# Kernel optimization log

Measured on AMD Instinct MI355X. Metric: run time of the kernel, lower is better.

## Reference

```python
import jax, jax.numpy as jnp
import numpy as np

N, F, E = 65536, 64, 16   # batch, fields, embedding_size
H1, H2 = 8, 4             # hidden_dims
BN_EPS = 1e-5


def setup_inputs() -> dict:
    key = jax.random.key(0)
    ks = jax.random.split(key, 12)
    rn = lambda k, shape, sc=1.0: jax.random.normal(k, shape, dtype=jnp.float32) * sc
    return {
        "Xa": rn(ks[0], (N, F)),
        "Xc": rn(ks[1], (N, F)),
        # per-field Linear(1,1) weights/biases (two first-order embedding lists)
        "w1": rn(ks[2], (F,)), "b1": rn(ks[3], (F,)),
        "w2": rn(ks[4], (F,)), "b2": rn(ks[5], (F,)),
        # per-field Linear(1,E) weights/biases (two second-order embedding lists)
        "W1": rn(ks[6], (F, E)), "B1": rn(ks[7], (F, E)),
        "W2": rn(ks[8], (F, E)), "B2": rn(ks[9], (F, E)),
        # deep MLP: linear_1 (F*E -> 8) + BN, linear_2 (8 -> 4). No final layer (init bug).
        "lin1_w": rn(ks[10], (H1, F * E), 0.01), "lin1_b": jnp.zeros((H1,), jnp.float32),
        "bn1_gamma": jnp.ones((H1,), jnp.float32), "bn1_beta": jnp.zeros((H1,), jnp.float32),
        "lin2_w": rn(ks[11], (H2, H1), 0.01), "lin2_b": jnp.full((H2,), 0.21, jnp.float32),
    }


def reference(Xa, Xc, w1, b1, w2, b2, W1, B1, W2, B2,
              lin1_w, lin1_b, bn1_gamma, bn1_beta, lin2_w, lin2_b):
    n = Xa.shape[0]
    # ---- FM first order (faithful to the torch broadcast: arr_2[i] is (N,N)
    # with entry [r,c] = Xa[r,i]*(w2[i]*Xc[c,i]+b2[i]); only mean over the
    # concat dim is consumed, so compute the column-mean analytically). ----
    first1 = (w1 * Xa + b1) * Xc                         # (N,F)
    xc_mean = jnp.mean(Xc, axis=0)                       # (F,)
    first2_cmean = Xa * (w2 * xc_mean + b2)              # (N,F) = mean over c of arr_2
    fm_first_mean = jnp.mean(first1 + first2_cmean, axis=1, keepdims=True)  # (N,1)

    # ---- FM second order: per-field (N,E) embeddings, fully batched. ----
    Xa3 = Xa[:, :, None]                                 # (N,F,1)
    Xc3 = Xc[:, :, None]
    emb = (Xa3 * W1 + B1) * Xc3 + Xa3 * (W2 * Xc3 + B2)  # (N,F,E)
    s = emb.sum(axis=1)                                  # (N,E)
    fm_second = 0.5 * (s * s - (emb * emb).sum(axis=1))  # (N,E)
    fm_second_mean = jnp.mean(fm_second, axis=1, keepdims=True)  # (N,1)

    # ---- deep part: cat of per-field (N,E) -> (N, F*E), field-major. ----
    deep = emb.reshape(n, F * E)
    h = deep @ lin1_w.T + lin1_b                         # (N,8)
    mu = h.mean(axis=0)
    var = h.var(axis=0)                                  # biased, as BN training mode
    h = (h - mu) / jnp.sqrt(var + BN_EPS) * bn1_gamma + bn1_beta
    h = jnp.tanh(h)                                      # dropout = identity (eval)
    h = h @ lin2_w.T + lin2_b                            # (N,4) — no final projection (init bug)
    deep_mean = h.mean(axis=1, keepdims=True)            # (N,1)

    return fm_first_mean + fm_second_mean + deep_mean    # (N,1)
```

## Files before the change

kernel.cpp:

```cpp
#include <hip/hip_runtime.h>
#include <math.h>

#define NROWS 65536
#define BN_EPS 1e-5f
#define NBLK   512

#define OFF_PARTIAL 0
#define OFF_H       65536
#define OFF_REC     589824
#define OFF_BLKT    595200
#define OFF_T       636160

__global__ __launch_bounds__(64) void precompute_kernel(
    const float* __restrict__ W1, const float* __restrict__ B1,
    const float* __restrict__ W2, const float* __restrict__ B2,
    const float* __restrict__ lin1_w, const float* __restrict__ w1,
    const float* __restrict__ b1, const float* __restrict__ b2,
    float* __restrict__ rec)
{
    int f = blockIdx.x, t = threadIdx.x;
    __shared__ float u[16], x[16], y[16];
    if (t < 16) {
        float uu = W1[f * 16 + t] + W2[f * 16 + t];
        float xx = B1[f * 16 + t];
        float yy = B2[f * 16 + t];
        u[t] = uu; x[t] = xx; y[t] = yy;
        rec[f * 84 + t]      = uu;
        rec[f * 84 + 16 + t] = xx;
        rec[f * 84 + 32 + t] = yy;
    }
    __syncthreads();
    if (t < 24) {
        int j = t & 7, which = t >> 3;
        const float* src = (which == 0) ? u : (which == 1) ? x : y;
        const float* lw = lin1_w + j * 1024 + f * 16;
        float acc = 0.f;
#pragma unroll
        for (int e = 0; e < 16; e++) acc = fmaf(src[e], lw[e], acc);
        rec[f * 84 + 48 + which * 8 + j] = acc;
    } else if (t < 30) {
        int q = t - 24;
        const float* s1 = (q == 0 || q == 3 || q == 4) ? u : (q == 1 || q == 5) ? x : y;
        const float* s2 = (q == 0) ? u : (q == 1 || q == 3) ? x : y;
        float acc = 0.f;
#pragma unroll
        for (int e = 0; e < 16; e++) acc = fmaf(s1[e], s2[e], acc);
        rec[f * 84 + 72 + q] = (q < 3 ? 1.f : 2.f) * acc;
    } else if (t == 30) {
        rec[f * 84 + 78] = w1[f];
        rec[f * 84 + 79] = b1[f];
        rec[f * 84 + 80] = b2[f];
        rec[f * 84 + 81] = 0.f;
        rec[f * 84 + 82] = 0.f;
        rec[f * 84 + 83] = 0.f;
    }
}

__global__ __launch_bounds__(256, 4) void main_kernel(
    const float* __restrict__ Xa, const float* __restrict__ Xc,
    const float* __restrict__ rec, const float* __restrict__ lin1_b,
    float* __restrict__ ws_partial, float* __restrict__ ws_h,
    float* __restrict__ ws_blkT)
{
    __shared__ float cmb[4][64][29];
    __shared__ float scol[256];

    int tid  = threadIdx.x;
    int lane = tid & 63;
    int wv   = tid >> 6;
    int wu   = __builtin_amdgcn_readfirstlane(wv);
    int blk  = blockIdx.x;
    int f0   = wu * 16;
    int rowbase = blk * 128;

    {
        int col = tid & 63, grp = tid >> 6;
        float acc = 0.f;
        for (int r = grp; r < 128; r += 4)
            acc += Xc[(size_t)(rowbase + r) * 64 + col];
        scol[tid] = acc;
    }
    __syncthreads();
    if (tid < 64) {
        float t = scol[tid] + scol[64 + tid] + scol[128 + tid] + scol[192 + tid];
        ws_blkT[(size_t)tid * NBLK + blk] = t;
    }

    size_t rb0 = ((size_t)rowbase + lane) * 64 + f0;
    const float4* pa0 = (const float4*)(Xa + rb0);
    const float4* pc0 = (const float4*)(Xc + rb0);
    const float4* pa1 = (const float4*)(Xa + rb0 + 64 * 64);
    const float4* pc1 = (const float4*)(Xc + rb0 + 64 * 64);

    float s0[16], s1[16], h0[8], h1[8];
#pragma unroll
    for (int e = 0; e < 16; e++) { s0[e] = 0.f; s1[e] = 0.f; }
#pragma unroll
    for (int j = 0; j < 8; j++) { h0[j] = 0.f; h1[j] = 0.f; }
    float p1a = 0.f, p1b = 0.f, p2a0 = 0.f, p2a1 = 0.f, q0 = 0.f, q1 = 0.f;

    const float* recw = rec + (size_t)f0 * 84;
#pragma unroll
    for (int k = 0; k < 4; k++) {
        float4 A0 = pa0[k], C0 = pc0[k];
        float4 A1 = pa1[k], C1 = pc1[k];
        float av0[4] = {A0.x, A0.y, A0.z, A0.w};
        float cv0[4] = {C0.x, C0.y, C0.z, C0.w};
        float av1[4] = {A1.x, A1.y, A1.z, A1.w};
        float cv1[4] = {C1.x, C1.y, C1.z, C1.w};
#pragma unroll
        for (int uu = 0; uu < 4; uu++) {
            const float* r = recw + (k * 4 + uu) * 84;
            {
                float a = av0[uu], c = cv0[uu], pp = a * c;
                p1a  = fmaf(fmaf(r[78], a, r[79]), c, p1a);
                p2a0 = fmaf(a, r[80], p2a0);
                q0 = fmaf(pp * pp, r[72], q0);
                q0 = fmaf(c * c,   r[73], q0);
                q0 = fmaf(a * a,   r[74], q0);
                q0 = fmaf(pp * c,  r[75], q0);
                q0 = fmaf(pp * a,  r[76], q0);
                q0 = fmaf(pp,      r[77], q0);
#pragma unroll
                for (int e = 0; e < 16; e++)
                    s0[e] = fmaf(pp, r[e], fmaf(c, r[16+e], fmaf(a, r[32+e], s0[e])));
#pragma unroll
                for (int j = 0; j < 8; j++)
                    h0[j] = fmaf(pp, r[48+j], fmaf(c, r[56+j], fmaf(a, r[64+j], h0[j])));
            }
            {
                float a = av1[uu], c = cv1[uu], pp = a * c;
                p1b  = fmaf(fmaf(r[78], a, r[79]), c, p1b);
                p2a1 = fmaf(a, r[80], p2a1);
                q1 = fmaf(pp * pp, r[72], q1);
                q1 = fmaf(c * c,   r[73], q1);
                q1 = fmaf(a * a,   r[74], q1);
                q1 = fmaf(pp * c,  r[75], q1);
                q1 = fmaf(pp * a,  r[76], q1);
                q1 = fmaf(pp,      r[77], q1);
#pragma unroll
                for (int e = 0; e < 16; e++)
                    s1[e] = fmaf(pp, r[e], fmaf(c, r[16+e], fmaf(a, r[32+e], s1[e])));
#pragma unroll
                for (int j = 0; j < 8; j++)
                    h1[j] = fmaf(pp, r[48+j], fmaf(c, r[56+j], fmaf(a, r[64+j], h1[j])));
            }
        }
    }

    float bn[16];
#pragma unroll
    for (int i = 0; i < 16; i++) bn[i] = 0.f;

#pragma unroll
    for (int g = 0; g < 2; g++) {
        __syncthreads();
#pragma unroll
        for (int e = 0; e < 16; e++) cmb[wv][lane][e] = g ? s1[e] : s0[e];
#pragma unroll
        for (int j = 0; j < 8; j++) cmb[wv][lane][16 + j] = g ? h1[j] : h0[j];
        cmb[wv][lane][24] = g ? p1b : p1a;
        cmb[wv][lane][25] = g ? p2a1 : p2a0;
        cmb[wv][lane][26] = g ? q1 : q0;
        __syncthreads();

        if (tid < 64) {
            float S[16], H[8], P1 = 0.f, P2 = 0.f, Q = 0.f;
#pragma unroll
            for (int e = 0; e < 16; e++) S[e] = 0.f;
#pragma unroll
            for (int j = 0; j < 8; j++) H[j] = 0.f;
#pragma unroll
            for (int w = 0; w < 4; w++) {
#pragma unroll
                for (int e = 0; e < 16; e++) S[e] += cmb[w][tid][e];
#pragma unroll
                for (int j = 0; j < 8; j++) H[j] += cmb[w][tid][16 + j];
                P1 += cmb[w][tid][24];
                P2 += cmb[w][tid][25];
                Q  += cmb[w][tid][26];
            }
#pragma unroll
            for (int j = 0; j < 8; j++) H[j] += lin1_b[j];

            float ss = 0.f;
#pragma unroll
            for (int e = 0; e < 16; e++) ss = fmaf(S[e], S[e], ss);
            int rr = rowbase + g * 64 + tid;
            ws_partial[rr] = (P1 + P2) * (1.f / 64.f) + (ss - Q) * (0.5f / 16.f);
            *(float4*)(ws_h + (size_t)rr * 8)     = make_float4(H[0], H[1], H[2], H[3]);
            *(float4*)(ws_h + (size_t)rr * 8 + 4) = make_float4(H[4], H[5], H[6], H[7]);
#pragma unroll
            for (int j = 0; j < 8; j++) {
                bn[j]     += H[j];
                bn[8 + j] += H[j] * H[j];
            }
        }
    }

    if (tid < 64) {
#pragma unroll
        for (int off = 1; off < 64; off <<= 1) {
#pragma unroll
            for (int i = 0; i < 16; i++) bn[i] += __shfl_xor(bn[i], off);
        }
        if (tid == 0) {
#pragma unroll
            for (int i = 0; i < 16; i++)
                ws_blkT[(size_t)(64 + i) * NBLK + blk] = bn[i];
        }
    }
}

__global__ __launch_bounds__(256) void reduce_kernel(
    const float* __restrict__ ws_blkT, float* __restrict__ T)
{
    int gtid = blockIdx.x * 256 + threadIdx.x;
    int v = gtid >> 6;
    int lane = gtid & 63;
    const float* p = ws_blkT + (size_t)v * NBLK + lane;
    float acc = 0.f;
#pragma unroll
    for (int k = 0; k < 8; k++) acc += p[k * 64];
#pragma unroll
    for (int off = 32; off; off >>= 1) acc += __shfl_xor(acc, off);
    if (lane == 0) T[v] = acc;
}

__global__ __launch_bounds__(256) void final_kernel(
    const float* __restrict__ Xa, const float* __restrict__ w2,
    const float* __restrict__ gamma, const float* __restrict__ beta,
    const float* __restrict__ lin2_w, const float* __restrict__ lin2_b,
    const float* __restrict__ T, const float* __restrict__ ws_partial,
    const float* __restrict__ ws_h, float* __restrict__ out)
{
    __shared__ float sg[64], sScale[8], sShift[8], sColw[8];
    __shared__ float sBsum;
    int tid = threadIdx.x;
    if (tid < 64) {
        sg[tid] = w2[tid] * (T[tid] * (1.f / 65536.f));
    } else if (tid < 72) {
        int j = tid - 64;
        float mu  = T[64 + j] * (1.f / 65536.f);
        float var = T[72 + j] * (1.f / 65536.f) - mu * mu;
        float sc = gamma[j] / sqrtf(var + BN_EPS);
        sScale[j] = sc;
        sShift[j] = beta[j] - mu * sc;
    } else if (tid < 80) {
        int j = tid - 72;
        sColw[j] = lin2_w[j] + lin2_w[8 + j] + lin2_w[16 + j] + lin2_w[24 + j];
    } else if (tid == 80) {
        sBsum = lin2_b[0] + lin2_b[1] + lin2_b[2] + lin2_b[3];
    }
    __syncthreads();

    int row  = (blockIdx.x * 256 + tid) >> 1;
    int half = tid & 1;
    int fo   = half * 32;

    const float4* xa4 = (const float4*)(Xa + (size_t)row * 64 + fo);
    float p2b = 0.f;
#pragma unroll
    for (int k = 0; k < 8; k++) {
        float4 vv = xa4[k];
        int b = fo + k * 4;
        p2b += vv.x * sg[b] + vv.y * sg[b + 1] + vv.z * sg[b + 2] + vv.w * sg[b + 3];
    }

    float4 hq = *(const float4*)(ws_h + (size_t)row * 8 + half * 4);
    float hv[4] = {hq.x, hq.y, hq.z, hq.w};
    float dmp = 0.f;
#pragma unroll
    for (int jj = 0; jj < 4; jj++) {
        int j = half * 4 + jj;
        float hn = tanhf(hv[jj] * sScale[j] + sShift[j]);
        dmp = fmaf(hn, sColw[j], dmp);
    }

    float val = p2b * (1.f / 64.f) + dmp * 0.25f;
    val += __shfl_xor(val, 1);
    if (!half)
        out[row] = val + ws_partial[row] + sBsum * 0.25f;
}

extern "C" void kernel_launch(void* const* d_in, const int* in_sizes, int n_in,
                              void* d_out, int out_size, void* d_ws, size_t ws_size,
                              hipStream_t stream) {
    const float* Xa        = (const float*)d_in[0];
    const float* Xc        = (const float*)d_in[1];
    const float* w1        = (const float*)d_in[2];
    const float* b1        = (const float*)d_in[3];
    const float* w2        = (const float*)d_in[4];
    const float* b2        = (const float*)d_in[5];
    const float* W1        = (const float*)d_in[6];
    const float* B1        = (const float*)d_in[7];
    const float* W2        = (const float*)d_in[8];
    const float* B2        = (const float*)d_in[9];
    const float* lin1_w    = (const float*)d_in[10];
    const float* lin1_b    = (const float*)d_in[11];
    const float* bn1_gamma = (const float*)d_in[12];
    const float* bn1_beta  = (const float*)d_in[13];
    const float* lin2_w    = (const float*)d_in[14];
    const float* lin2_b    = (const float*)d_in[15];

    float* ws  = (float*)d_ws;
    float* out = (float*)d_out;

    float* ws_partial = ws + OFF_PARTIAL;
    float* ws_h       = ws + OFF_H;
    float* ws_rec     = ws + OFF_REC;
    float* ws_blkT    = ws + OFF_BLKT;
    float* ws_T       = ws + OFF_T;

    precompute_kernel<<<64, 64, 0, stream>>>(W1, B1, W2, B2, lin1_w,
                                             w1, b1, b2, ws_rec);
    main_kernel<<<NBLK, 256, 0, stream>>>(Xa, Xc, ws_rec, lin1_b,
                                          ws_partial, ws_h, ws_blkT);
    reduce_kernel<<<20, 256, 0, stream>>>(ws_blkT, ws_T);
    final_kernel<<<512, 256, 0, stream>>>(Xa, w2, bn1_gamma, bn1_beta,
                                          lin2_w, lin2_b, ws_T,
                                          ws_partial, ws_h, out);
}
```

Measured before the change: 129.2 us.

## Recast per-row field contractions as bf16 MFMA GEMM against precomputed fragments

Replaces the per-thread fp32 FMA loops over fields with a bf16 MFMA GEMM. Each row's features (a·c, c, a, and the quadratic terms) are packed as bf16 into LDS and multiplied against a precomputed bf16 B-fragment matrix that holds the embedding weights, the lin1 projections and the quadratic-norm coefficients. Block size drops to 64 rows and the grid doubles, and the reduce kernel is adjusted to match. This is meant to cut VALU work, but bf16 rounding of the inputs and weights loosens accuracy, especially for the squared-norm terms that are later subtracted.

```diff
diff --git a/kernel.cpp b/kernel.cpp
--- a/kernel.cpp
+++ b/kernel.cpp
@@ -3,80 +3,107 @@
 
 #define NROWS 65536
 #define BN_EPS 1e-5f
-#define NBLK   512
+#define NBLK   1024
+
+typedef __attribute__((ext_vector_type(8))) short bf16x8;
+typedef __attribute__((ext_vector_type(4))) float f32x4;
 
 #define OFF_PARTIAL 0
 #define OFF_H       65536
-#define OFF_REC     589824
-#define OFF_BLKT    595200
-#define OFF_T       636160
-
-__global__ __launch_bounds__(64) void precompute_kernel(
-    const float* __restrict__ W1, const float* __restrict__ B1,
-    const float* __restrict__ W2, const float* __restrict__ B2,
+#define OFF_BF      589824
+#define OFF_BLKT    598016
+#define OFF_T       679936
+
+__device__ inline unsigned short f2bf(float x) {
+    union { float f; unsigned u; } v; v.f = x;
+    unsigned u = v.u;
+    u += 0x7FFFu + ((u >> 16) & 1u);
+    return (unsigned short)(u >> 16);
+}
+
+__global__ __launch_bounds__(64) void bfrag_kernel(
+    const float* __restrict__ W1, const float* __restrict__ B1g,
+    const float* __restrict__ W2, const float* __restrict__ B2g,
     const float* __restrict__ lin1_w, const float* __restrict__ w1,
     const float* __restrict__ b1, const float* __restrict__ b2,
-    float* __restrict__ rec)
+    unsigned short* __restrict__ Bf)
 {
-    int f = blockIdx.x, t = threadIdx.x;
-    __shared__ float u[16], x[16], y[16];
-    if (t < 16) {
-        float uu = W1[f * 16 + t] + W2[f * 16 + t];
-        float xx = B1[f * 16 + t];
-        float yy = B2[f * 16 + t];
-        u[t] = uu; x[t] = xx; y[t] = yy;
-        rec[f * 84 + t]      = uu;
-        rec[f * 84 + 16 + t] = xx;
-        rec[f * 84 + 32 + t] = yy;
-    }
-    __syncthreads();
-    if (t < 24) {
-        int j = t & 7, which = t >> 3;
-        const float* src = (which == 0) ? u : (which == 1) ? x : y;
-        const float* lw = lin1_w + j * 1024 + f * 16;
-        float acc = 0.f;
-#pragma unroll
-        for (int e = 0; e < 16; e++) acc = fmaf(src[e], lw[e], acc);
-        rec[f * 84 + 48 + which * 8 + j] = acc;
-    } else if (t < 30) {
-        int q = t - 24;
-        const float* s1 = (q == 0 || q == 3 || q == 4) ? u : (q == 1 || q == 5) ? x : y;
-        const float* s2 = (q == 0) ? u : (q == 1 || q == 3) ? x : y;
-        float acc = 0.f;
-#pragma unroll
-        for (int e = 0; e < 16; e++) acc = fmaf(s1[e], s2[e], acc);
-        rec[f * 84 + 72 + q] = (q < 3 ? 1.f : 2.f) * acc;
-    } else if (t == 30) {
-        rec[f * 84 + 78] = w1[f];
-        rec[f * 84 + 79] = b1[f];
-        rec[f * 84 + 80] = b2[f];
-        rec[f * 84 + 81] = 0.f;
-        rec[f * 84 + 82] = 0.f;
-        rec[f * 84 + 83] = 0.f;
-    }
-}
-
-__global__ __launch_bounds__(256, 4) void main_kernel(
+    int i    = blockIdx.x;
+    int gkc  = i >> 1;
+    int nt   = i & 1;
+    int lane = threadIdx.x;
+    int quad = lane >> 4;
+    int n    = nt * 16 + (lane & 15);
+
+    unsigned short outv[8];
+#pragma unroll
+    for (int j = 0; j < 8; j++) {
+        int k = gkc * 32 + quad * 8 + j;
+        int b = k >> 6, f = k & 63;
+        float v = 0.f;
+        if (n < 16) {
+            if (b == 0)      v = W1[f * 16 + n] + W2[f * 16 + n];
+            else if (b == 1) v = B1g[f * 16 + n];
+            else if (b == 2) v = B2g[f * 16 + n];
+        } else if (n < 24) {
+            if (b < 3) {
+                const float* lw = lin1_w + (n - 16) * 1024 + f * 16;
+                float acc = 0.f;
+                for (int e = 0; e < 16; e++) {
+                    float src = (b == 0) ? (W1[f * 16 + e] + W2[f * 16 + e])
+                              : (b == 1) ? B1g[f * 16 + e] : B2g[f * 16 + e];
+                    acc = fmaf(src, lw[e], acc);
+                }
+                v = acc;
+            }
+        } else if (n == 24) {
+            if (b == 0 || b >= 3) {
+                float acc = 0.f;
+                for (int e = 0; e < 16; e++) {
+                    float U = W1[f * 16 + e] + W2[f * 16 + e];
+                    float x = B1g[f * 16 + e], y = B2g[f * 16 + e];
+                    float t = (b == 0) ? x * y : (b == 3) ? U * U : (b == 4) ? x * x
+                            : (b == 5) ? y * y : (b == 6) ? U * x : U * y;
+                    acc += t;
+                }
+                v = (b == 0 || b == 6 || b == 7) ? 2.f * acc : acc;
+            }
+        } else if (n == 25) {
+            if (b == 0)      v = w1[f];
+            else if (b == 1) v = b1[f];
+        } else if (n == 26) {
+            if (b == 2) v = b2[f];
+        }
+        outv[j] = f2bf(v);
+    }
+    unsigned u[4];
+#pragma unroll
+    for (int p = 0; p < 4; p++)
+        u[p] = (unsigned)outv[2 * p] | ((unsigned)outv[2 * p + 1] << 16);
+    uint4* dst = (uint4*)(Bf + (size_t)((gkc * 2 + nt) * 64 + lane) * 8);
+    *dst = make_uint4(u[0], u[1], u[2], u[3]);
+}
+
+__global__ __launch_bounds__(256) void main_kernel(
     const float* __restrict__ Xa, const float* __restrict__ Xc,
-    const float* __restrict__ rec, const float* __restrict__ lin1_b,
+    const unsigned short* __restrict__ Bf, const float* __restrict__ lin1_b,
     float* __restrict__ ws_partial, float* __restrict__ ws_h,
     float* __restrict__ ws_blkT)
 {
-    __shared__ float cmb[4][64][29];
+    __shared__ unsigned sL[64 * 132];
+    __shared__ float sD[64][33];
     __shared__ float scol[256];
 
     int tid  = threadIdx.x;
     int lane = tid & 63;
     int wv   = tid >> 6;
-    int wu   = __builtin_amdgcn_readfirstlane(wv);
     int blk  = blockIdx.x;
-    int f0   = wu * 16;
-    int rowbase = blk * 128;
+    int rowbase = blk * 64;
 
     {
         int col = tid & 63, grp = tid >> 6;
         float acc = 0.f;
-        for (int r = grp; r < 128; r += 4)
+        for (int r = grp; r < 64; r += 4)
             acc += Xc[(size_t)(rowbase + r) * 64 + col];
         scol[tid] = acc;
     }
@@ -86,119 +113,91 @@
         ws_blkT[(size_t)tid * NBLK + blk] = t;
     }
 
-    size_t rb0 = ((size_t)rowbase + lane) * 64 + f0;
-    const float4* pa0 = (const float4*)(Xa + rb0);
-    const float4* pc0 = (const float4*)(Xc + rb0);
-    const float4* pa1 = (const float4*)(Xa + rb0 + 64 * 64);
-    const float4* pc1 = (const float4*)(Xc + rb0 + 64 * 64);
-
-    float s0[16], s1[16], h0[8], h1[8];
-#pragma unroll
-    for (int e = 0; e < 16; e++) { s0[e] = 0.f; s1[e] = 0.f; }
-#pragma unroll
-    for (int j = 0; j < 8; j++) { h0[j] = 0.f; h1[j] = 0.f; }
-    float p1a = 0.f, p1b = 0.f, p2a0 = 0.f, p2a1 = 0.f, q0 = 0.f, q1 = 0.f;
-
-    const float* recw = rec + (size_t)f0 * 84;
+    int r_local = tid >> 2, qt = tid & 3;
+    size_t rbase = ((size_t)rowbase + r_local) * 64 + qt * 16;
+    const float4* pa = (const float4*)(Xa + rbase);
+    const float4* pc = (const float4*)(Xc + rbase);
+    float a_[16], c_[16];
 #pragma unroll
     for (int k = 0; k < 4; k++) {
-        float4 A0 = pa0[k], C0 = pc0[k];
-        float4 A1 = pa1[k], C1 = pc1[k];
-        float av0[4] = {A0.x, A0.y, A0.z, A0.w};
-        float cv0[4] = {C0.x, C0.y, C0.z, C0.w};
-        float av1[4] = {A1.x, A1.y, A1.z, A1.w};
-        float cv1[4] = {C1.x, C1.y, C1.z, C1.w};
-#pragma unroll
-        for (int uu = 0; uu < 4; uu++) {
-            const float* r = recw + (k * 4 + uu) * 84;
-            {
-                float a = av0[uu], c = cv0[uu], pp = a * c;
-                p1a  = fmaf(fmaf(r[78], a, r[79]), c, p1a);
-                p2a0 = fmaf(a, r[80], p2a0);
-                q0 = fmaf(pp * pp, r[72], q0);
-                q0 = fmaf(c * c,   r[73], q0);
-                q0 = fmaf(a * a,   r[74], q0);
-                q0 = fmaf(pp * c,  r[75], q0);
-                q0 = fmaf(pp * a,  r[76], q0);
-                q0 = fmaf(pp,      r[77], q0);
-#pragma unroll
-                for (int e = 0; e < 16; e++)
-                    s0[e] = fmaf(pp, r[e], fmaf(c, r[16+e], fmaf(a, r[32+e], s0[e])));
-#pragma unroll
-                for (int j = 0; j < 8; j++)
-                    h0[j] = fmaf(pp, r[48+j], fmaf(c, r[56+j], fmaf(a, r[64+j], h0[j])));
+        float4 av = pa[k], cv = pc[k];
+        a_[k*4] = av.x; a_[k*4+1] = av.y; a_[k*4+2] = av.z; a_[k*4+3] = av.w;
+        c_[k*4] = cv.x; c_[k*4+1] = cv.y; c_[k*4+2] = cv.z; c_[k*4+3] = cv.w;
+    }
+
+    int quad = lane >> 4, m = lane & 15;
+    const bf16x8* aptr = (const bf16x8*)(sL + (wv * 16 + m) * 132 + quad * 4);
+    const bf16x8* bptr = (const bf16x8*)Bf;
+
+    f32x4 acc0 = {0.f, 0.f, 0.f, 0.f};
+    f32x4 acc1 = {0.f, 0.f, 0.f, 0.f};
+
+#pragma unroll
+    for (int pass = 0; pass < 2; pass++) {
+        __syncthreads();
+        unsigned ub[4][8];
+#pragma unroll
+        for (int e = 0; e < 16; e++) {
+            float a = a_[e], c = c_[e], pp = a * c;
+            float v4[4];
+            if (pass == 0) { v4[0] = pp;    v4[1] = c;     v4[2] = a;      v4[3] = pp * pp; }
+            else           { v4[0] = c * c; v4[1] = a * a; v4[2] = pp * c; v4[3] = pp * a; }
+#pragma unroll
+            for (int bl = 0; bl < 4; bl++) {
+                unsigned short h = f2bf(v4[bl]);
+                if ((e & 1) == 0) ub[bl][e >> 1] = h;
+                else              ub[bl][e >> 1] |= ((unsigned)h << 16);
             }
-            {
-                float a = av1[uu], c = cv1[uu], pp = a * c;
-                p1b  = fmaf(fmaf(r[78], a, r[79]), c, p1b);
-                p2a1 = fmaf(a, r[80], p2a1);
-                q1 = fmaf(pp * pp, r[72], q1);
-                q1 = fmaf(c * c,   r[73], q1);
-                q1 = fmaf(a * a,   r[74], q1);
-                q1 = fmaf(pp * c,  r[75], q1);
-                q1 = fmaf(pp * a,  r[76], q1);
-                q1 = fmaf(pp,      r[77], q1);
-#pragma unroll
-                for (int e = 0; e < 16; e++)
-                    s1[e] = fmaf(pp, r[e], fmaf(c, r[16+e], fmaf(a, r[32+e], s1[e])));
-#pragma unroll
-                for (int j = 0; j < 8; j++)
-                    h1[j] = fmaf(pp, r[48+j], fmaf(c, r[56+j], fmaf(a, r[64+j], h1[j])));
-            }
-        }
-    }
-
-    float bn[16];
-#pragma unroll
-    for (int i = 0; i < 16; i++) bn[i] = 0.f;
-
-#pragma unroll
-    for (int g = 0; g < 2; g++) {
+        }
+#pragma unroll
+        for (int bl = 0; bl < 4; bl++) {
+            unsigned* dst = sL + r_local * 132 + bl * 32 + qt * 8;
+            ((uint4*)dst)[0] = make_uint4(ub[bl][0], ub[bl][1], ub[bl][2], ub[bl][3]);
+            ((uint4*)dst)[1] = make_uint4(ub[bl][4], ub[bl][5], ub[bl][6], ub[bl][7]);
+        }
         __syncthreads();
-#pragma unroll
-        for (int e = 0; e < 16; e++) cmb[wv][lane][e] = g ? s1[e] : s0[e];
-#pragma unroll
-        for (int j = 0; j < 8; j++) cmb[wv][lane][16 + j] = g ? h1[j] : h0[j];
-        cmb[wv][lane][24] = g ? p1b : p1a;
-        cmb[wv][lane][25] = g ? p2a1 : p2a0;
-        cmb[wv][lane][26] = g ? q1 : q0;
-        __syncthreads();
-
-        if (tid < 64) {
-            float S[16], H[8], P1 = 0.f, P2 = 0.f, Q = 0.f;
-#pragma unroll
-            for (int e = 0; e < 16; e++) S[e] = 0.f;
-#pragma unroll
-            for (int j = 0; j < 8; j++) H[j] = 0.f;
-#pragma unroll
-            for (int w = 0; w < 4; w++) {
-#pragma unroll
-                for (int e = 0; e < 16; e++) S[e] += cmb[w][tid][e];
-#pragma unroll
-                for (int j = 0; j < 8; j++) H[j] += cmb[w][tid][16 + j];
-                P1 += cmb[w][tid][24];
-                P2 += cmb[w][tid][25];
-                Q  += cmb[w][tid][26];
-            }
-#pragma unroll
-            for (int j = 0; j < 8; j++) H[j] += lin1_b[j];
-
-            float ss = 0.f;
-#pragma unroll
-            for (int e = 0; e < 16; e++) ss = fmaf(S[e], S[e], ss);
-            int rr = rowbase + g * 64 + tid;
-            ws_partial[rr] = (P1 + P2) * (1.f / 64.f) + (ss - Q) * (0.5f / 16.f);
-            *(float4*)(ws_h + (size_t)rr * 8)     = make_float4(H[0], H[1], H[2], H[3]);
-            *(float4*)(ws_h + (size_t)rr * 8 + 4) = make_float4(H[4], H[5], H[6], H[7]);
-#pragma unroll
-            for (int j = 0; j < 8; j++) {
-                bn[j]     += H[j];
-                bn[8 + j] += H[j] * H[j];
-            }
-        }
-    }
+
+#pragma unroll 2
+        for (int kc = 0; kc < 8; kc++) {
+            int gkc = pass * 8 + kc;
+            bf16x8 af = aptr[kc * 4];
+            bf16x8 b0 = bptr[(size_t)(gkc * 2) * 64 + lane];
+            bf16x8 b1 = bptr[(size_t)(gkc * 2 + 1) * 64 + lane];
+            acc0 = __builtin_amdgcn_mfma_f32_16x16x32_bf16(af, b0, acc0, 0, 0, 0);
+            acc1 = __builtin_amdgcn_mfma_f32_16x16x32_bf16(af, b1, acc1, 0, 0, 0);
+        }
+    }
+
+    __syncthreads();
+#pragma unroll
+    for (int reg = 0; reg < 4; reg++) {
+        int rowD = wv * 16 + quad * 4 + reg;
+        sD[rowD][m]      = acc0[reg];
+        sD[rowD][16 + m] = acc1[reg];
+    }
+    __syncthreads();
 
     if (tid < 64) {
+        float S[16], H[8];
+#pragma unroll
+        for (int e = 0; e < 16; e++) S[e] = sD[tid][e];
+#pragma unroll
+        for (int j = 0; j < 8; j++) H[j] = sD[tid][16 + j] + lin1_b[j];
+        float q   = sD[tid][24];
+        float p1  = sD[tid][25];
+        float p2a = sD[tid][26];
+
+        float ss = 0.f;
+#pragma unroll
+        for (int e = 0; e < 16; e++) ss = fmaf(S[e], S[e], ss);
+        int rr = rowbase + tid;
+        ws_partial[rr] = (p1 + p2a) * (1.f / 64.f) + (ss - q) * (0.5f / 16.f);
+        *(float4*)(ws_h + (size_t)rr * 8)     = make_float4(H[0], H[1], H[2], H[3]);
+        *(float4*)(ws_h + (size_t)rr * 8 + 4) = make_float4(H[4], H[5], H[6], H[7]);
+
+        float bn[16];
+#pragma unroll
+        for (int j = 0; j < 8; j++) { bn[j] = H[j]; bn[8 + j] = H[j] * H[j]; }
 #pragma unroll
         for (int off = 1; off < 64; off <<= 1) {
 #pragma unroll
@@ -221,7 +220,7 @@
     const float* p = ws_blkT + (size_t)v * NBLK + lane;
     float acc = 0.f;
 #pragma unroll
-    for (int k = 0; k < 8; k++) acc += p[k * 64];
+    for (int k = 0; k < 16; k++) acc += p[k * 64];
 #pragma unroll
     for (int off = 32; off; off >>= 1) acc += __shfl_xor(acc, off);
     if (lane == 0) T[v] = acc;
@@ -306,15 +305,15 @@
     float* ws  = (float*)d_ws;
     float* out = (float*)d_out;
 
-    float* ws_partial = ws + OFF_PARTIAL;
-    float* ws_h       = ws + OFF_H;
-    float* ws_rec     = ws + OFF_REC;
-    float* ws_blkT    = ws + OFF_BLKT;
-    float* ws_T       = ws + OFF_T;
-
-    precompute_kernel<<<64, 64, 0, stream>>>(W1, B1, W2, B2, lin1_w,
-                                             w1, b1, b2, ws_rec);
-    main_kernel<<<NBLK, 256, 0, stream>>>(Xa, Xc, ws_rec, lin1_b,
+    float* ws_partial       = ws + OFF_PARTIAL;
+    float* ws_h             = ws + OFF_H;
+    unsigned short* ws_bf   = (unsigned short*)(ws + OFF_BF);
+    float* ws_blkT          = ws + OFF_BLKT;
+    float* ws_T             = ws + OFF_T;
+
+    bfrag_kernel<<<32, 64, 0, stream>>>(W1, B1, W2, B2, lin1_w,
+                                        w1, b1, b2, ws_bf);
+    main_kernel<<<NBLK, 256, 0, stream>>>(Xa, Xc, ws_bf, lin1_b,
                                           ws_partial, ws_h, ws_blkT);
     reduce_kernel<<<20, 256, 0, stream>>>(ws_blkT, ws_T);
     final_kernel<<<512, 256, 0, stream>>>(Xa, w2, bn1_gamma, bn1_beta,
```

Measured after the change: 155.4 us. 1.2x slower.
